# Kernel tuning notes

Hardware: AMD Instinct MI355X
Metric: run time of the kernel (lower is better)

The kernel has to match this reference:

```python
import jax, jax.numpy as jnp
import numpy as np

B, D, U, HU = 2048, 1024, 1024, 256

def _ln(x, eps=1e-3):
    # Keras LayerNormalization(center=False, scale=False), default epsilon=1e-3
    m = jnp.mean(x, axis=-1, keepdims=True)
    v = jnp.var(x, axis=-1, keepdims=True)
    return (x - m) * jax.lax.rsqrt(v + eps)

def setup_inputs() -> dict:
    key = jax.random.key(0)
    ks = jax.random.split(key, 17)
    s = 0.02
    return {
        "inputs": jax.random.normal(ks[0], (B, D), jnp.float32),
        "main_h": 0.1 * jax.random.normal(ks[1], (B, U), jnp.float32),
        "main_c": 0.1 * jax.random.normal(ks[2], (B, U), jnp.float32),
        "hyper_h": 0.1 * jax.random.normal(ks[3], (B, HU), jnp.float32),
        "hyper_c": 0.1 * jax.random.normal(ks[4], (B, HU), jnp.float32),
        "kernel": s * jax.random.normal(ks[5], (D, 4 * U), jnp.float32),
        "recurrent_kernel": s * jax.random.normal(ks[6], (U, 4 * U), jnp.float32),
        "bias": jnp.zeros((4 * U,), jnp.float32),
        "hyper_kernel": s * jax.random.normal(ks[7], (D + U, 4 * HU), jnp.float32),
        "hyper_rec_kernel": s * jax.random.normal(ks[8], (HU, 4 * HU), jnp.float32),
        "hyper_bias": jnp.zeros((4 * HU,), jnp.float32),
        "dx_w": s * jax.random.normal(ks[9], (HU, 4 * U), jnp.float32),
        "dx_b": s * jax.random.normal(ks[10], (4 * U,), jnp.float32),
        "dh_w": s * jax.random.normal(ks[11], (HU, 4 * U), jnp.float32),
        "dh_b": s * jax.random.normal(ks[12], (4 * U,), jnp.float32),
        "db_w": s * jax.random.normal(ks[13], (HU, 4 * U), jnp.float32),
        "db_b": s * jax.random.normal(ks[14], (4 * U,), jnp.float32),
    }

def reference(inputs, main_h, main_c, hyper_h, hyper_c,
              kernel, recurrent_kernel, bias,
              hyper_kernel, hyper_rec_kernel, hyper_bias,
              dx_w, dx_b, dh_w, dh_b, db_w, db_b):
    # --- hyper LSTMCell (Keras gate order i, f, g, o) ---
    hx = jnp.concatenate([inputs, main_h], axis=-1)          # [B, D+U]
    z = hx @ hyper_kernel + hyper_h @ hyper_rec_kernel + hyper_bias  # [B, 4*HU]
    hi, hf, hg, ho = jnp.split(z, 4, axis=-1)
    hyper_c_new = jax.nn.sigmoid(hf) * hyper_c + jax.nn.sigmoid(hi) * jnp.tanh(hg)
    hyper_out = jax.nn.sigmoid(ho) * jnp.tanh(hyper_c_new)  # = hyper_h_new

    # --- hypernet gate scalings ---
    d_x = hyper_out @ dx_w + dx_b                            # [B, 4*U]
    d_h = hyper_out @ dh_w + dh_b
    d_b = hyper_out @ db_w + db_b

    # --- main LSTM gates with hyper modulation + LayerNorm ---
    proj_x = inputs @ kernel + bias                          # [B, 4*U]
    proj_h = main_h @ recurrent_kernel                       # [B, 4*U]
    gates = _ln(d_x * proj_x + d_h * proj_h + d_b)
    i, f, g, o = jnp.split(gates, 4, axis=-1)
    main_c_new = jax.nn.sigmoid(f) * main_c + jax.nn.sigmoid(i) * jnp.tanh(g)
    main_h_new = jax.nn.sigmoid(o) * jnp.tanh(_ln(main_c_new))
    return (main_h_new, main_c_new, hyper_out, hyper_c_new)
```

## Files before the change

kernel.cpp:

```cpp
#include <hip/hip_runtime.h>
#include <cstdint>

typedef unsigned short u16;
typedef _Float16 half8 __attribute__((ext_vector_type(8)));
typedef float floatx4 __attribute__((ext_vector_type(4)));
typedef unsigned short ushort8v __attribute__((ext_vector_type(8)));
typedef unsigned short ushort4v __attribute__((ext_vector_type(4)));
typedef float float4v __attribute__((ext_vector_type(4)));

#define BB 2048
#define UU 1024
#define HUx 256
#define O_H  0
#define O_C  (BB*UU)
#define O_HO (2*BB*UU)
#define O_HC (2*BB*UU + BB*HUx)
#define MFMAH __builtin_amdgcn_mfma_f32_16x16x32_f16

#define LBAR() do { \
    asm volatile("s_waitcnt lgkmcnt(0)\n\ts_barrier" ::: "memory"); \
    __builtin_amdgcn_sched_barrier(0); \
} while (0)

__device__ __forceinline__ float bf2f(u16 u) {
    union { uint32_t i; float f; } v; v.i = ((uint32_t)u) << 16; return v.f;
}
__device__ __forceinline__ u16 f2bf(float f) {
    union { float f; uint32_t i; } v; v.f = f;
    uint32_t r = v.i + 0x7fffu + ((v.i >> 16) & 1u);
    return (u16)(r >> 16);
}
__device__ __forceinline__ u16 f2h(float f) {
    _Float16 h = (_Float16)f; u16 u; __builtin_memcpy(&u, &h, 2); return u;
}
__device__ __forceinline__ float sigf(float x) { return 1.f / (1.f + expf(-x)); }
__device__ __forceinline__ float ldmix(const void* p, size_t i, int isbf) {
    return isbf ? bf2f(((const u16*)p)[i]) : ((const float*)p)[i];
}
__device__ __forceinline__ u16 ld2h(const void* p, size_t i, int isbf) {
    return f2h(ldmix(p, i, isbf));
}

__device__ __forceinline__ void ld128(half8 r[2], const u16* src, int row0, int ldK,
                                      int k0, int tid) {
    #pragma unroll
    for (int i = 0; i < 2; i++) {
        int v = tid + 256 * i;
        r[i] = *(const half8*)(src + (size_t)(row0 + (v >> 2)) * ldK + k0 + (v & 3) * 8);
    }
}
__device__ __forceinline__ void ld64(half8& r, const u16* src, int row0, int ldK,
                                     int k0, int tid) {
    r = *(const half8*)(src + (size_t)(row0 + (tid >> 2)) * ldK + k0 + (tid & 3) * 8);
}
__device__ __forceinline__ void wrS128(u16* lds, const half8 r[2], int tid) {
    #pragma unroll
    for (int i = 0; i < 2; i++) {
        int v = tid + 256 * i;
        int ps = (v & 3) ^ ((v >> 3) & 3);
        *(half8*)&lds[(v >> 2) * 32 + ps * 8] = r[i];
    }
}
__device__ __forceinline__ void wrS64(u16* lds, half8 r, int tid) {
    int ps = (tid & 3) ^ ((tid >> 3) & 3);
    *(half8*)&lds[(tid >> 2) * 32 + ps * 8] = r;
}

__device__ __forceinline__ int detect_local(const u16* raw) {
    int lane = threadIdx.x & 63;
    u16 u = raw[2 * lane];
    int e = (u >> 7) & 0xFF;
    unsigned long long m = __ballot(e >= 100 && e <= 134);
    return (__popcll(m) >= 32) ? 1 : 0;
}

__device__ __forceinline__ void transpose_tile_v(const void* in, u16* out, int C,
                                                 int ostride, int ocol, int r0, int c0,
                                                 int isbf, u16* th ) {
    int tid = threadIdx.x;
    int ty = tid >> 3, tx4 = (tid & 7) * 4;
    ushort4v v;
    if (isbf) {
        ushort4v q = *(const ushort4v*)((const u16*)in + (size_t)(r0 + ty) * C + c0 + tx4);
        #pragma unroll
        for (int j = 0; j < 4; j++) v[j] = f2h(bf2f(q[j]));
    } else {
        float4v q = *(const float4v*)((const float*)in + (size_t)(r0 + ty) * C + c0 + tx4);
        #pragma unroll
        for (int j = 0; j < 4; j++) v[j] = f2h(q[j]);
    }
    *(ushort4v*)&th[ty * 36 + tx4] = v;
    __syncthreads();
    ushort4v w;
    #pragma unroll
    for (int j = 0; j < 4; j++) w[j] = th[(tx4 + j) * 36 + ty];
    *(ushort4v*)(out + (size_t)(c0 + ty) * ostride + ocol + r0 + tx4) = w;
}

__global__ __launch_bounds__(256) void prep_in(
    const void* __restrict__ xs, const void* __restrict__ ms, const void* __restrict__ hs,
    const void* __restrict__ hyper_k, const void* __restrict__ hyper_rk,
    u16* __restrict__ xh, u16* __restrict__ mh, u16* __restrict__ hh,
    u16* __restrict__ BTh, int* __restrict__ flag) {
    __shared__ __align__(16) u16 th[32 * 36];
    int bid = blockIdx.x, tid = threadIdx.x;
    int isbf = detect_local((const u16*)xs);
    if (bid == 0 && tid == 0) *flag = isbf;

    if (bid < 2304) {
        int i = bid * 256 + tid;
        const void* src; u16* dst; int t;
        if (i < 262144)      { src = xs; dst = xh; t = i; }
        else if (i < 524288) { src = ms; dst = mh; t = i - 262144; }
        else                 { src = hs; dst = hh; t = i - 524288; }
        half8 o;
        if (isbf) {
            ushort8v v = *(const ushort8v*)((const u16*)src + (size_t)t * 8);
            #pragma unroll
            for (int j = 0; j < 8; j++) o[j] = (_Float16)bf2f(v[j]);
        } else {
            float4v a = *(const float4v*)((const float*)src + (size_t)t * 8);
            float4v b = *(const float4v*)((const float*)src + (size_t)t * 8 + 4);
            #pragma unroll
            for (int j = 0; j < 4; j++) { o[j] = (_Float16)a[j]; o[j + 4] = (_Float16)b[j]; }
        }
        *(half8*)(dst + (size_t)t * 8) = o;
    } else if (bid < 4352) {
        int u = bid - 2304;
        transpose_tile_v(hyper_k, BTh, 1024, 2304, 0, (u >> 5) * 32, (u & 31) * 32, isbf, th);
    } else {
        int u = bid - 4352;
        transpose_tile_v(hyper_rk, BTh, 1024, 2304, 2048, (u >> 5) * 32, (u & 31) * 32, isbf, th);
    }
}

__global__ __launch_bounds__(256) void gemm_cell_wt(
    const u16* __restrict__ xh, const u16* __restrict__ mh, const u16* __restrict__ hh,
    const u16* __restrict__ BT,
    const void* __restrict__ xs, const void* __restrict__ hyper_c,
    const void* __restrict__ hyper_b, void* __restrict__ out, u16* __restrict__ ho16,
    const void* __restrict__ kernel_w, const void* __restrict__ rec_w,
    const void* __restrict__ dx_w, const void* __restrict__ dh_w,
    const void* __restrict__ db_w,
    u16* __restrict__ kT, u16* __restrict__ rkT,
    u16* __restrict__ dxT, u16* __restrict__ dhT, u16* __restrict__ dbT) {
    __shared__ __align__(16) u16 S[2][8192];
    int bid = blockIdx.x, tid = threadIdx.x;

    if (bid >= 128) {
        int isbf = detect_local((const u16*)xs);
        int u = bid - 128;
        const void* in; u16* outT; int ostride, r0, c0;
        if (u < 8192) {
            in  = (u < 4096) ? kernel_w : rec_w;
            outT = (u < 4096) ? kT : rkT;
            int r = u & 4095;
            ostride = 1024; r0 = (r >> 7) * 32; c0 = (r & 127) * 32;
        } else {
            int v = u - 8192;
            int zi = v >> 10, r = v & 1023;
            in  = (zi == 0) ? dx_w : (zi == 1) ? dh_w : db_w;
            outT = (zi == 0) ? dxT : (zi == 1) ? dhT : dbT;
            ostride = 256; r0 = (r >> 7) * 32; c0 = (r & 127) * 32;
        }
        transpose_tile_v(in, outT, 4096, ostride, 0, r0, c0, isbf, (u16*)S);
        return;
    }

    int isbf = detect_local((const u16*)xs);
    int lane = tid & 63, wave = tid >> 6;
    int wm = (wave & 1) * 64, ws = wave >> 1;
    int bx = bid & 7, by = bid >> 3;
    int bm = by * 128;
    int mr = lane & 15;
    int kqs = ((lane >> 4) ^ ((mr >> 1) & 3)) * 8;
    floatx4 acc[4][4] = {};

    half8 nA[2], nB[2];

    #define LDA_S(R, S_) do { \
        int s_ = (S_); \
        const u16* Ap_; int ldA_, kA_; \
        if (s_ < 32)      { Ap_ = xh; ldA_ = 1024; kA_ = s_ * 32; } \
        else if (s_ < 64) { Ap_ = mh; ldA_ = 1024; kA_ = (s_ - 32) * 32; } \
        else              { Ap_ = hh; ldA_ = 256;  kA_ = (s_ - 64) * 32; } \
        ld128(R, Ap_, bm, ldA_, kA_, tid); \
    } while (0)
    #define LDB_S(R, S_) do { \
        int s_ = (S_); \
        _Pragma("unroll") \
        for (int i_ = 0; i_ < 2; i_++) { \
            int v_ = tid + 256 * i_; \
            int br_ = v_ >> 2; \
            int col_ = ((br_ & 63) >> 4) * 256 + (bx * 2 + (br_ >> 6)) * 16 + (br_ & 15); \
            (R)[i_] = *(const half8*)(BT + (size_t)col_ * 2304 + s_ * 32 + (v_ & 3) * 8); \
        } \
    } while (0)

    LDA_S(nA, 0); LDB_S(nB, 0);
    wrS128(S[0], nA, tid); wrS128(S[0] + 4096, nB, tid);
    LDA_S(nA, 1); LDB_S(nB, 1);
    LBAR();

    #pragma unroll 1
    for (int s = 0; s < 72; s++) {
        int p = s & 1;
        const u16* C = S[p];
        u16* N = S[p ^ 1];
        half8 a[4], b[4];
        #pragma unroll
        for (int t = 0; t < 4; t++)
            a[t] = *(const half8*)&C[(wm + t * 16 + mr) * 32 + kqs];
        #pragma unroll
        for (int t = 0; t < 4; t++)
            b[t] = *(const half8*)&C[4096 + (ws * 64 + t * 16 + mr) * 32 + kqs];
        if (s < 71) {
            wrS128(N, nA, tid); wrS128(N + 4096, nB, tid);
            if (s < 70) { LDA_S(nA, s + 2); LDB_S(nB, s + 2); }
        }
        #pragma unroll
        for (int tm = 0; tm < 4; tm++)
            #pragma unroll
            for (int tn = 0; tn < 4; tn++)
                acc[tm][tn] = MFMAH(a[tm], b[tn], acc[tm][tn], 0, 0, 0);
        LBAR();
    }
    #undef LDA_S
    #undef LDB_S

    int hu = (bx * 2 + ws) * 16 + mr;
    float bi = ldmix(hyper_b, hu, isbf);
    float bf = ldmix(hyper_b, hu + 256, isbf);
    float bg = ldmix(hyper_b, hu + 512, isbf);
    float bo = ldmix(hyper_b, hu + 768, isbf);
    #pragma unroll
    for (int tm = 0; tm < 4; tm++) {
        #pragma unroll
        for (int rr = 0; rr < 4; rr++) {
            int row = bm + wm + tm * 16 + (lane >> 4) * 4 + rr;
            size_t idx = (size_t)row * 256 + hu;
            float hi = acc[tm][0][rr] + bi;
            float hf = acc[tm][1][rr] + bf;
            float hg = acc[tm][2][rr] + bg;
            float hoo = acc[tm][3][rr] + bo;
            float c = ldmix(hyper_c, idx, isbf);
            float cn = sigf(hf) * c + sigf(hi) * tanhf(hg);
            float hout = sigf(hoo) * tanhf(cn);
            ho16[idx] = f2h(hout);
            if (isbf) {
                ((u16*)out)[O_HO + idx] = f2bf(hout);
                ((u16*)out)[O_HC + idx] = f2bf(cn);
            } else {
                ((float*)out)[O_HO + idx] = hout;
                ((float*)out)[O_HC + idx] = cn;
            }
        }
    }
}

__global__ __launch_bounds__(256, 2) void mega_fused(
    const u16* __restrict__ xh, const u16* __restrict__ mh, const u16* __restrict__ ho16,
    const u16* __restrict__ kT, const u16* __restrict__ rkT,
    const u16* __restrict__ dxT, const u16* __restrict__ dhT, const u16* __restrict__ dbT,
    const void* __restrict__ bias, const void* __restrict__ dx_b,
    const void* __restrict__ dh_b, const void* __restrict__ db_b,
    u16* __restrict__ gp, const int* __restrict__ flag) {
    __shared__ __align__(16) u16 S[2][12288];
    int isbf = *flag;
    int tid = threadIdx.x, lane = tid & 63, wave = tid >> 6;
    int wm = (wave & 1) * 64, wn = (wave >> 1) * 32;
    int bm = blockIdx.y * 128, bn = blockIdx.x * 64;
    floatx4 apx[4][2] = {}, aph[4][2] = {}, adx[4][2] = {}, adh[4][2] = {}, adb[4][2] = {};
    int mr = lane & 15;
    int kqs = (((lane >> 4) ^ ((mr >> 1) & 3))) * 8;

    half8 nA1[2], nA2[2], nB1, nB2, nB3;

    ld128(nA1, xh,  bm, 1024, 0, tid);
    ld128(nA2, mh,  bm, 1024, 0, tid);
    ld64(nB1, kT,  bn, 1024, 0, tid);
    ld64(nB2, rkT, bn, 1024, 0, tid);
    wrS128(S[0], nA1, tid); wrS128(S[0] + 4096, nA2, tid);
    wrS64(S[0] + 8192, nB1, tid); wrS64(S[0] + 10240, nB2, tid);
    ld128(nA1, xh,  bm, 1024, 32, tid);
    ld128(nA2, mh,  bm, 1024, 32, tid);
    ld64(nB1, kT,  bn, 1024, 32, tid);
    ld64(nB2, rkT, bn, 1024, 32, tid);
    LBAR();

    #pragma unroll 1
    for (int k0 = 0; k0 < 1024; k0 += 32) {
        int p = (k0 >> 5) & 1;
        const u16* C = S[p];
        u16* N = S[p ^ 1];
        half8 ax[4], am[4], bk[2], br[2];
        #pragma unroll
        for (int t = 0; t < 4; t++) {
            int ra = (wm + t * 16 + mr) * 32 + kqs;
            ax[t] = *(const half8*)&C[ra];
            am[t] = *(const half8*)&C[4096 + ra];
        }
        #pragma unroll
        for (int t = 0; t < 2; t++) {
            int rb = (wn + t * 16 + mr) * 32 + kqs;
            bk[t] = *(const half8*)&C[8192 + rb];
            br[t] = *(const half8*)&C[10240 + rb];
        }
        if (k0 < 992) {
            wrS128(N, nA1, tid); wrS128(N + 4096, nA2, tid);
            wrS64(N + 8192, nB1, tid); wrS64(N + 10240, nB2, tid);
        } else {
            wrS128(N, nA1, tid);
            wrS64(N + 8192, nB1, tid); wrS64(N + 10240, nB2, tid); wrS64(N + 4096, nB3, tid);
        }
        if (k0 < 960) {
            ld128(nA1, xh,  bm, 1024, k0 + 64, tid);
            ld128(nA2, mh,  bm, 1024, k0 + 64, tid);
            ld64(nB1, kT,  bn, 1024, k0 + 64, tid);
            ld64(nB2, rkT, bn, 1024, k0 + 64, tid);
        } else if (k0 == 960) {
            ld128(nA1, ho16, bm, 256, 0, tid);
            ld64(nB1, dxT, bn, 256, 0, tid);
            ld64(nB2, dhT, bn, 256, 0, tid);
            ld64(nB3, dbT, bn, 256, 0, tid);
        } else {
            ld128(nA1, ho16, bm, 256, 32, tid);
            ld64(nB1, dxT, bn, 256, 32, tid);
            ld64(nB2, dhT, bn, 256, 32, tid);
            ld64(nB3, dbT, bn, 256, 32, tid);
        }
        #pragma unroll
        for (int tm = 0; tm < 4; tm++)
            #pragma unroll
            for (int tn = 0; tn < 2; tn++) {
                apx[tm][tn] = MFMAH(ax[tm], bk[tn], apx[tm][tn], 0, 0, 0);
                aph[tm][tn] = MFMAH(am[tm], br[tn], aph[tm][tn], 0, 0, 0);
            }
        LBAR();
    }

    #pragma unroll 1
    for (int k0 = 0; k0 < 256; k0 += 32) {
        int p = (k0 >> 5) & 1;
        const u16* C = S[p];
        u16* N = S[p ^ 1];
        half8 a[4], bx[2], bh[2], bb[2];
        #pragma unroll
        for (int t = 0; t < 4; t++) {
            int ra = (wm + t * 16 + mr) * 32 + kqs;
            a[t] = *(const half8*)&C[ra];
        }
        #pragma unroll
        for (int t = 0; t < 2; t++) {
            int rb = (wn + t * 16 + mr) * 32 + kqs;
            bx[t] = *(const half8*)&C[8192 + rb];
            bh[t] = *(const half8*)&C[10240 + rb];
            bb[t] = *(const half8*)&C[4096 + rb];
        }
        if (k0 < 224) {
            wrS128(N, nA1, tid);
            wrS64(N + 8192, nB1, tid); wrS64(N + 10240, nB2, tid); wrS64(N + 4096, nB3, tid);
        }
        if (k0 < 192) {
            ld128(nA1, ho16, bm, 256, k0 + 64, tid);
            ld64(nB1, dxT, bn, 256, k0 + 64, tid);
            ld64(nB2, dhT, bn, 256, k0 + 64, tid);
            ld64(nB3, dbT, bn, 256, k0 + 64, tid);
        }
        #pragma unroll
        for (int tm = 0; tm < 4; tm++)
            #pragma unroll
            for (int tn = 0; tn < 2; tn++) {
                adx[tm][tn] = MFMAH(a[tm], bx[tn], adx[tm][tn], 0, 0, 0);
                adh[tm][tn] = MFMAH(a[tm], bh[tn], adh[tm][tn], 0, 0, 0);
                adb[tm][tn] = MFMAH(a[tm], bb[tn], adb[tm][tn], 0, 0, 0);
            }
        LBAR();
    }

    #pragma unroll
    for (int tn = 0; tn < 2; tn++) {
        int col = bn + wn + tn * 16 + (lane & 15);
        float bv  = ldmix(bias, col, isbf);
        float dxb = ldmix(dx_b, col, isbf);
        float dhb = ldmix(dh_b, col, isbf);
        float dbb = ldmix(db_b, col, isbf);
        #pragma unroll
        for (int tm = 0; tm < 4; tm++) {
            #pragma unroll
            for (int rr = 0; rr < 4; rr++) {
                int row = bm + wm + tm * 16 + (lane >> 4) * 4 + rr;
                float px = apx[tm][tn][rr] + bv;
                float ph = aph[tm][tn][rr];
                float dx = adx[tm][tn][rr] + dxb;
                float dh = adh[tm][tn][rr] + dhb;
                float db = adb[tm][tn][rr] + dbb;
                gp[(size_t)row * 4096 + col] = f2h(dx * px + dh * ph + db);
            }
        }
    }
}

__device__ __forceinline__ void block_reduce2(float& a, float& b, float* red) {
    #pragma unroll
    for (int o = 32; o > 0; o >>= 1) {
        a += __shfl_down(a, o, 64);
        b += __shfl_down(b, o, 64);
    }
    int lane = threadIdx.x & 63, w = threadIdx.x >> 6;
    if (lane == 0) { red[w] = a; red[4 + w] = b; }
    __syncthreads();
    a = red[0] + red[1] + red[2] + red[3];
    b = red[4] + red[5] + red[6] + red[7];
    __syncthreads();
}

__global__ __launch_bounds__(256) void ln_main(const u16* __restrict__ gp,
                                               const void* __restrict__ main_c,
                                               void* __restrict__ out,
                                               const int* __restrict__ flag) {
    __shared__ float sPre[4096];
    __shared__ float sC[1024];
    __shared__ float red[8];
    int isbf = *flag;
    int b = blockIdx.x, tid = threadIdx.x;
    const u16* g = gp + (size_t)b * 4096;
    float s = 0.f, q = 0.f;
    for (int j0 = tid * 8; j0 < 4096; j0 += 2048) {
        half8 v = *(const half8*)(g + j0);
        #pragma unroll
        for (int e = 0; e < 8; e++) {
            float f = (float)v[e];
            sPre[j0 + e] = f; s += f; q += f * f;
        }
    }
    block_reduce2(s, q, red);
    float mean = s * (1.f / 4096.f);
    float var = q * (1.f / 4096.f) - mean * mean;
    float rs = rsqrtf(var + 1e-3f);
    float s2 = 0.f, q2 = 0.f;
    for (int u = tid; u < 1024; u += 256) {
        float gi = (sPre[u] - mean) * rs;
        float gf = (sPre[u + 1024] - mean) * rs;
        float gg = (sPre[u + 2048] - mean) * rs;
        float c = ldmix(main_c, (size_t)b * 1024 + u, isbf);
        float cn = sigf(gf) * c + sigf(gi) * tanhf(gg);
        sC[u] = cn;
        if (isbf) ((u16*)out)[O_C + (size_t)b * 1024 + u] = f2bf(cn);
        else      ((float*)out)[O_C + (size_t)b * 1024 + u] = cn;
        s2 += cn; q2 += cn * cn;
    }
    block_reduce2(s2, q2, red);
    float m2 = s2 * (1.f / 1024.f);
    float v2 = q2 * (1.f / 1024.f) - m2 * m2;
    float rs2 = rsqrtf(v2 + 1e-3f);
    for (int u = tid; u < 1024; u += 256) {
        float go = (sPre[u + 3072] - mean) * rs;
        float hn = sigf(go) * tanhf((sC[u] - m2) * rs2);
        if (isbf) ((u16*)out)[O_H + (size_t)b * 1024 + u] = f2bf(hn);
        else      ((float*)out)[O_H + (size_t)b * 1024 + u] = hn;
    }
}

extern "C" void kernel_launch(void* const* d_in, const int* in_sizes, int n_in,
                              void* d_out, int out_size, void* d_ws, size_t ws_size,
                              hipStream_t stream) {
    (void)in_sizes; (void)n_in; (void)out_size; (void)ws_size;
    const void* inputs   = d_in[0];
    const void* main_h   = d_in[1];
    const void* main_c   = d_in[2];
    const void* hyper_h  = d_in[3];
    const void* hyper_c  = d_in[4];
    const void* kernel_w = d_in[5];
    const void* rec_w    = d_in[6];
    const void* bias     = d_in[7];
    const void* hyper_k  = d_in[8];
    const void* hyper_rk = d_in[9];
    const void* hyper_b  = d_in[10];
    const void* dx_w = d_in[11];
    const void* dx_b = d_in[12];
    const void* dh_w = d_in[13];
    const void* dh_b = d_in[14];
    const void* db_w = d_in[15];
    const void* db_b = d_in[16];
    char* ws = (char*)d_ws;
    const size_t MB = 1024 * 1024;

    int* flag = (int*)ws;
    size_t off = 256;
    u16* xh  = (u16*)(ws + off); off += 4 * MB;
    u16* mh  = (u16*)(ws + off); off += 4 * MB;
    u16* hh  = (u16*)(ws + off); off += 1 * MB;
    u16* ho  = (u16*)(ws + off); off += 1 * MB;
    u16* kT  = (u16*)(ws + off); off += 8 * MB;
    u16* rkT = (u16*)(ws + off); off += 8 * MB;
    u16* dxT = (u16*)(ws + off); off += 2 * MB;
    u16* dhT = (u16*)(ws + off); off += 2 * MB;
    u16* dbT = (u16*)(ws + off); off += 2 * MB;
    u16* BTh = (u16*)(ws + off); off += (size_t)1024 * 2304 * 2;
    u16* gp  = (u16*)(ws + off); off += 16 * MB;

    prep_in<<<4608, 256, 0, stream>>>(inputs, main_h, hyper_h, hyper_k, hyper_rk,
                                      xh, mh, hh, BTh, flag);
    gemm_cell_wt<<<128 + 11264, 256, 0, stream>>>(xh, mh, hh, BTh,
                                                  inputs, hyper_c, hyper_b, d_out, ho,
                                                  kernel_w, rec_w, dx_w, dh_w, db_w,
                                                  kT, rkT, dxT, dhT, dbT);
    mega_fused<<<dim3(64, 16), 256, 0, stream>>>(xh, mh, ho, kT, rkT, dxT, dhT, dbT,
                                                 bias, dx_b, dh_b, db_b, gp, flag);
    ln_main<<<2048, 256, 0, stream>>>(gp, main_c, d_out, flag);
}
```

Before: 271.4 us.

## Split hyper-LSTM GEMM K-loop across wave pairs with LDS reduction, doubling blocks

The hyper gate GEMM now launches 256 tiles instead of 128. Each tile covers 64 columns (16 hidden units × 4 gates) rather than 128. Within a block, the two wave pairs split the 72-step K loop into halves of 36, each with its own double-buffered LDS region. Their partial accumulators are summed through LDS before the LSTM-cell epilogue. This targets low occupancy, since 128 blocks underfill the GPU's compute units, at the cost of more LDS, an extra reduction, duplicated B loads and only half the threads doing the epilogue.

```diff
diff --git a/kernel.cpp b/kernel.cpp
--- a/kernel.cpp
+++ b/kernel.cpp
@@ -144,12 +144,12 @@
     const void* __restrict__ db_w,
     u16* __restrict__ kT, u16* __restrict__ rkT,
     u16* __restrict__ dxT, u16* __restrict__ dhT, u16* __restrict__ dbT) {
-    __shared__ __align__(16) u16 S[2][8192];
+    __shared__ __align__(16) u16 S[2][2][6144];
     int bid = blockIdx.x, tid = threadIdx.x;
 
-    if (bid >= 128) {
+    if (bid >= 256) {
         int isbf = detect_local((const u16*)xs);
-        int u = bid - 128;
+        int u = bid - 256;
         const void* in; u16* outT; int ostride, r0, c0;
         if (u < 8192) {
             in  = (u < 4096) ? kernel_w : rec_w;
@@ -169,54 +169,76 @@
 
     int isbf = detect_local((const u16*)xs);
     int lane = tid & 63, wave = tid >> 6;
-    int wm = (wave & 1) * 64, ws = wave >> 1;
-    int bx = bid & 7, by = bid >> 3;
+    int wm = (wave & 1) * 64, wk = wave >> 1;
+    int t128 = tid & 127;
+    int sx = bid & 15, by = bid >> 4;
     int bm = by * 128;
     int mr = lane & 15;
     int kqs = ((lane >> 4) ^ ((mr >> 1) & 3)) * 8;
+    int sBase = wk * 36;
     floatx4 acc[4][4] = {};
 
-    half8 nA[2], nB[2];
-
-    #define LDA_S(R, S_) do { \
+    half8 nA[4], nB[2];
+
+    #define LDA_H(R, S_) do { \
         int s_ = (S_); \
         const u16* Ap_; int ldA_, kA_; \
         if (s_ < 32)      { Ap_ = xh; ldA_ = 1024; kA_ = s_ * 32; } \
         else if (s_ < 64) { Ap_ = mh; ldA_ = 1024; kA_ = (s_ - 32) * 32; } \
         else              { Ap_ = hh; ldA_ = 256;  kA_ = (s_ - 64) * 32; } \
-        ld128(R, Ap_, bm, ldA_, kA_, tid); \
+        _Pragma("unroll") \
+        for (int i_ = 0; i_ < 4; i_++) { \
+            int v_ = t128 + 128 * i_; \
+            (R)[i_] = *(const half8*)(Ap_ + (size_t)(bm + (v_ >> 2)) * ldA_ + kA_ + (v_ & 3) * 8); \
+        } \
     } while (0)
-    #define LDB_S(R, S_) do { \
+    #define LDB_H(R, S_) do { \
         int s_ = (S_); \
         _Pragma("unroll") \
         for (int i_ = 0; i_ < 2; i_++) { \
-            int v_ = tid + 256 * i_; \
+            int v_ = t128 + 128 * i_; \
             int br_ = v_ >> 2; \
-            int col_ = ((br_ & 63) >> 4) * 256 + (bx * 2 + (br_ >> 6)) * 16 + (br_ & 15); \
+            int col_ = (br_ >> 4) * 256 + sx * 16 + (br_ & 15); \
             (R)[i_] = *(const half8*)(BT + (size_t)col_ * 2304 + s_ * 32 + (v_ & 3) * 8); \
         } \
     } while (0)
-
-    LDA_S(nA, 0); LDB_S(nB, 0);
-    wrS128(S[0], nA, tid); wrS128(S[0] + 4096, nB, tid);
-    LDA_S(nA, 1); LDB_S(nB, 1);
+    #define WRA_H(L, R) do { \
+        _Pragma("unroll") \
+        for (int i_ = 0; i_ < 4; i_++) { \
+            int v_ = t128 + 128 * i_; \
+            int ps_ = (v_ & 3) ^ ((v_ >> 3) & 3); \
+            *(half8*)&(L)[(v_ >> 2) * 32 + ps_ * 8] = (R)[i_]; \
+        } \
+    } while (0)
+    #define WRB_H(L, R) do { \
+        _Pragma("unroll") \
+        for (int i_ = 0; i_ < 2; i_++) { \
+            int v_ = t128 + 128 * i_; \
+            int ps_ = (v_ & 3) ^ ((v_ >> 3) & 3); \
+            *(half8*)&(L)[4096 + (v_ >> 2) * 32 + ps_ * 8] = (R)[i_]; \
+        } \
+    } while (0)
+
+    LDA_H(nA, sBase); LDB_H(nB, sBase);
+    WRA_H(S[wk][0], nA); WRB_H(S[wk][0], nB);
+    LDA_H(nA, sBase + 1); LDB_H(nB, sBase + 1);
     LBAR();
 
     #pragma unroll 1
-    for (int s = 0; s < 72; s++) {
-        int p = s & 1;
-        const u16* C = S[p];
-        u16* N = S[p ^ 1];
+    for (int j = 0; j < 36; j++) {
+        int p = j & 1;
+        const u16* C = S[wk][p];
+        u16* N = S[wk][p ^ 1];
         half8 a[4], b[4];
         #pragma unroll
         for (int t = 0; t < 4; t++)
             a[t] = *(const half8*)&C[(wm + t * 16 + mr) * 32 + kqs];
         #pragma unroll
         for (int t = 0; t < 4; t++)
-            b[t] = *(const half8*)&C[4096 + (ws * 64 + t * 16 + mr) * 32 + kqs];
-        if (s < 71) {
-            wrS128(N, nA, tid); wrS128(N + 4096, nB, tid);
-            if (s < 70) { LDA_S(nA, s + 2); LDB_S(nB, s + 2); }
+            b[t] = *(const half8*)&C[4096 + (t * 16 + mr) * 32 + kqs];
+        if (j < 35) {
+            WRA_H(N, nA); WRB_H(N, nB);
+            if (j < 34) { LDA_H(nA, sBase + j + 2); LDB_H(nB, sBase + j + 2); }
         }
         #pragma unroll
         for (int tm = 0; tm < 4; tm++)
@@ -225,34 +247,54 @@
                 acc[tm][tn] = MFMAH(a[tm], b[tn], acc[tm][tn], 0, 0, 0);
         LBAR();
     }
-    #undef LDA_S
-    #undef LDB_S
-
-    int hu = (bx * 2 + ws) * 16 + mr;
-    float bi = ldmix(hyper_b, hu, isbf);
-    float bf = ldmix(hyper_b, hu + 256, isbf);
-    float bg = ldmix(hyper_b, hu + 512, isbf);
-    float bo = ldmix(hyper_b, hu + 768, isbf);
-    #pragma unroll
-    for (int tm = 0; tm < 4; tm++) {
-        #pragma unroll
-        for (int rr = 0; rr < 4; rr++) {
-            int row = bm + wm + tm * 16 + (lane >> 4) * 4 + rr;
-            size_t idx = (size_t)row * 256 + hu;
-            float hi = acc[tm][0][rr] + bi;
-            float hf = acc[tm][1][rr] + bf;
-            float hg = acc[tm][2][rr] + bg;
-            float hoo = acc[tm][3][rr] + bo;
-            float c = ldmix(hyper_c, idx, isbf);
-            float cn = sigf(hf) * c + sigf(hi) * tanhf(hg);
-            float hout = sigf(hoo) * tanhf(cn);
-            ho16[idx] = f2h(hout);
-            if (isbf) {
-                ((u16*)out)[O_HO + idx] = f2bf(hout);
-                ((u16*)out)[O_HC + idx] = f2bf(cn);
-            } else {
-                ((float*)out)[O_HO + idx] = hout;
-                ((float*)out)[O_HC + idx] = cn;
+    #undef LDA_H
+    #undef LDB_H
+    #undef WRA_H
+    #undef WRB_H
+
+    float* red = (float*)S;
+    if (wk == 1) {
+        int t = tid - 128;
+        #pragma unroll
+        for (int tm = 0; tm < 4; tm++)
+            #pragma unroll
+            for (int tn = 0; tn < 4; tn++)
+                *(floatx4*)&red[t * 64 + (tm * 4 + tn) * 4] = acc[tm][tn];
+    }
+    __syncthreads();
+    if (wk == 0) {
+        #pragma unroll
+        for (int tm = 0; tm < 4; tm++)
+            #pragma unroll
+            for (int tn = 0; tn < 4; tn++)
+                acc[tm][tn] += *(const floatx4*)&red[tid * 64 + (tm * 4 + tn) * 4];
+
+        int hu = sx * 16 + mr;
+        float bi = ldmix(hyper_b, hu, isbf);
+        float bf = ldmix(hyper_b, hu + 256, isbf);
+        float bg = ldmix(hyper_b, hu + 512, isbf);
+        float bo = ldmix(hyper_b, hu + 768, isbf);
+        #pragma unroll
+        for (int tm = 0; tm < 4; tm++) {
+            #pragma unroll
+            for (int rr = 0; rr < 4; rr++) {
+                int row = bm + wm + tm * 16 + (lane >> 4) * 4 + rr;
+                size_t idx = (size_t)row * 256 + hu;
+                float hi = acc[tm][0][rr] + bi;
+                float hf = acc[tm][1][rr] + bf;
+                float hg = acc[tm][2][rr] + bg;
+                float hoo = acc[tm][3][rr] + bo;
+                float c = ldmix(hyper_c, idx, isbf);
+                float cn = sigf(hf) * c + sigf(hi) * tanhf(hg);
+                float hout = sigf(hoo) * tanhf(cn);
+                ho16[idx] = f2h(hout);
+                if (isbf) {
+                    ((u16*)out)[O_HO + idx] = f2bf(hout);
+                    ((u16*)out)[O_HC + idx] = f2bf(cn);
+                } else {
+                    ((float*)out)[O_HO + idx] = hout;
+                    ((float*)out)[O_HC + idx] = cn;
+                }
             }
         }
     }
@@ -502,7 +544,7 @@
 
     prep_in<<<4608, 256, 0, stream>>>(inputs, main_h, hyper_h, hyper_k, hyper_rk,
                                       xh, mh, hh, BTh, flag);
-    gemm_cell_wt<<<128 + 11264, 256, 0, stream>>>(xh, mh, hh, BTh,
+    gemm_cell_wt<<<256 + 11264, 256, 0, stream>>>(xh, mh, hh, BTh,
                                                   inputs, hyper_c, hyper_b, d_out, ho,
                                                   kernel_w, rec_w, dx_w, dh_w, db_w,
                                                   kT, rkT, dxT, dhT, dbT);
```

Measured after the change: 273.4 us. About the same (+0.7%).
